# Kernel optimization log

Measured on AMD Instinct MI355X. Metric: run time of the kernel, lower is better.

Reference implementation:

```python
import jax, jax.numpy as jnp
import numpy as np

L0, L1, L2 = 32, 16, 8
NS, NB = 512, 256
CUT = 7.0
N, E, G = 16384, 131072, 16
FEAT = L0 + 3 * L1 + 5 * L2  # 120


def setup_inputs() -> dict:
    key = jax.random.key(0)
    ks = jax.random.split(key, 16)
    rn = lambda k, s, sc=1.0: jax.random.normal(k, s, jnp.float32) * sc
    inp = {}
    inp['nodes'] = rn(ks[0], (N, FEAT))
    inp['pos'] = rn(ks[1], (N, 3)) * 5.0
    inp['cell'] = rn(ks[2], (G, 3, 3))
    inp['edge_shift'] = rn(ks[3], (E, 3))
    # tensor-product path weights (e3nn FullyConnectedTensorProduct, uvw mode)
    inp['W0'] = rn(ks[4], (L0, L0, NS))
    inp['W1'] = rn(ks[5], (L1, L1, NS))
    inp['W2'] = rn(ks[6], (L2, L2, NS))
    inp['ln_g'] = jnp.ones((NS,), jnp.float32)
    inp['ln_b'] = jnp.zeros((NS,), jnp.float32)
    inp['df_w1'] = rn(ks[7], (NB, 1024), NB ** -0.5)
    inp['df_b1'] = jnp.zeros((1024,), jnp.float32)
    inp['df_w2'] = rn(ks[8], (1024, NS), 1024 ** -0.5)
    inp['df_b2'] = jnp.zeros((NS,), jnp.float32)
    inp['mi_w1'] = rn(ks[9], (NS, 1024), NS ** -0.5)
    inp['mi_b1'] = jnp.zeros((1024,), jnp.float32)
    inp['mi_w2'] = rn(ks[10], (1024, 1024), 1024 ** -0.5)
    inp['mi_b2'] = jnp.zeros((1024,), jnp.float32)
    inp['mo_w'] = rn(ks[11], (1024, 1), 1024 ** -0.5)
    inp['mo_b'] = jnp.zeros((1,), jnp.float32)
    inp['edge_index'] = jax.random.randint(ks[12], (2, E), 0, N)
    inp['batch_vec'] = jnp.sort(jax.random.randint(ks[13], (N,), 0, G))
    return inp


def _split_irreps(x):
    x0 = x[:, :L0]                                   # (E, L0) scalars 0e
    x1 = x[:, L0:L0 + 3 * L1].reshape(-1, L1, 3)      # (E, L1, 3) vectors 1o
    x2 = x[:, L0 + 3 * L1:].reshape(-1, L2, 5)        # (E, L2, 5) 2e
    return x0, x1, x2


def reference(nodes, pos, cell, edge_shift, W0, W1, W2, ln_g, ln_b,
              df_w1, df_b1, df_w2, df_b2, mi_w1, mi_b1, mi_w2, mi_b2,
              mo_w, mo_b, edge_index, batch_vec):
    src, dst = edge_index[0], edge_index[1]
    # periodic-image translation vector per edge
    bcell = cell[batch_vec[src]]                      # (E,3,3)
    tvec = jnp.einsum('ei,eij->ej', edge_shift, bcell)
    radvec = pos[dst] - pos[src] + tvec               # (E,3)
    dist = jnp.linalg.norm(radvec, axis=1, keepdims=True)  # (E,1)
    r = 1.0 / (dist + 1e-6)
    # Bessel radial embedding with cutoff CUT, NB basis functions
    n = jnp.arange(1, NB + 1, dtype=jnp.float32)
    emb = jnp.sqrt(2.0 / CUT) * jnp.sin(n * jnp.pi * r / CUT) / r  # (E,NB)
    distfilter = jax.nn.silu(emb @ df_w1 + df_b1) @ df_w2 + df_b2  # (E,NS)

    # symmetrized fully-connected tensor product -> 0e scalars
    # 0.5*(tp(xs,xd)+tp(xd,xs)) == contraction of euv with symmetrized W
    xs0, xs1, xs2 = _split_irreps(nodes[src])
    xd0, xd1, xd2 = _split_irreps(nodes[dst])
    fan = jnp.sqrt(jnp.float32(L0 * L0 + L1 * L1 + L2 * L2))  # element path norm
    sym = lambda W: 0.5 * (W + W.transpose(1, 0, 2))
    e0 = jnp.einsum('eu,ev->euv', xs0, xd0)
    mixed = jnp.einsum('euv,uvw->ew', e0, sym(W0)) / fan
    e1 = jnp.einsum('eui,evi->euv', xs1, xd1)
    mixed = mixed + jnp.einsum('euv,uvw->ew', e1, sym(W1)) / (fan * jnp.sqrt(3.0))
    e2 = jnp.einsum('eui,evi->euv', xs2, xd2)
    mixed = mixed + jnp.einsum('euv,uvw->ew', e2, sym(W2)) / (fan * jnp.sqrt(5.0))

    # LayerNorm over numscalars
    mu = jnp.mean(mixed, axis=-1, keepdims=True)
    var = jnp.mean((mixed - mu) ** 2, axis=-1, keepdims=True)
    mixednorm = (mixed - mu) * jax.lax.rsqrt(var + 1e-5) * ln_g + ln_b

    reg = mixednorm * distfilter
    h = jax.nn.silu(reg @ mi_w1 + mi_b1)
    h = jax.nn.silu(h @ mi_w2 + mi_b2)
    return h @ mo_w + mo_b  # (E,1)
```

## Files before the change

kernel.cpp:

```cpp
#include <hip/hip_runtime.h>

#define EE 131072
#define NNODE 16384
#define FEAT 120
#define NS 512
#define NB 256
#define KCAT 1344

typedef unsigned short u16;
typedef __bf16 bf16x8 __attribute__((ext_vector_type(8)));
typedef float f32x4 __attribute__((ext_vector_type(4)));
typedef unsigned short ushort8 __attribute__((ext_vector_type(8)));

__device__ __forceinline__ float b2f(u16 u) {
  union { unsigned int i; float f; } x; x.i = ((unsigned int)u) << 16; return x.f;
}
__device__ __forceinline__ u16 f2b(float f) {
  union { float f; unsigned int i; } x; x.f = f;
  unsigned int lsb = (x.i >> 16) & 1u;
  x.i += 0x7fffu + lsb;
  return (u16)(x.i >> 16);
}
__device__ __forceinline__ u16 f2b_fast(float f) {
  __bf16 h = (__bf16)f;
  union { __bf16 h; u16 u; } x; x.h = h; return x.u;
}
__device__ __forceinline__ float rdany(const void* p, long i, int f32) {
  return f32 ? ((const float*)p)[i] : b2f(((const u16*)p)[i]);
}

__device__ __forceinline__ void gload16(const u16* g, u16* l) {
  __builtin_amdgcn_global_load_lds(
      (__attribute__((address_space(1))) void*)(u16*)g,
      (__attribute__((address_space(3))) void*)l, 16, 0, 0);
}

struct PrepArgs {
  long cum[20];
  const void* src[19];
  u16* dst[19];
  float* outf;
  int* flag;
  const u16* nodes;
};

__global__ __launch_bounds__(256) void megaprep(PrepArgs a) {
  __shared__ int scnt[4];
  {
    u16 v = a.nodes[threadIdx.x];
    int e = (v >> 7) & 0xFF;
    unsigned long long b = __ballot(e >= 0x48);
    if ((threadIdx.x & 63) == 0) scnt[threadIdx.x >> 6] = __popcll(b);
  }
  __syncthreads();
  const int f32 = (scnt[0] + scnt[1] + scnt[2] + scnt[3]) >= 16;
  if (blockIdx.x == 0 && threadIdx.x == 0) *a.flag = f32;

  long i = (long)blockIdx.x * 256 + threadIdx.x;
  const long total = a.cum[19];
  if (i < total) {
    int s = 0;
    while (i >= a.cum[s + 1]) s++;
    long local = i - a.cum[s];
    a.dst[s][local] = f32 ? f2b(((const float*)a.src[s])[local])
                          : ((const u16*)a.src[s])[local];
  } else {
    long j = i - total;
    if (j < EE) a.outf[j] = 0.f;
  }
}

struct WprepArgs {
  const u16* tin[4];
  u16* tout[4];
  const u16 *W0, *W1, *W2;
  u16* wcT;
};

__device__ __forceinline__ void do_transpose(const u16* in, u16* out, int R, int C, int rem) {
  __shared__ u16 tile[32][33];
  const int bx = C >> 5;
  const int c0 = (rem % bx) * 32, r0 = (rem / bx) * 32;
  const int tx = threadIdx.x & 31, ty = threadIdx.x >> 5;
  for (int i = 0; i < 32; i += 8) {
    int r = r0 + ty + i, c = c0 + tx;
    if (r < R && c < C) tile[ty + i][tx] = in[(long)r * C + c];
  }
  __syncthreads();
  for (int i = 0; i < 32; i += 8) {
    int r = r0 + tx, c = c0 + ty + i;
    if (r < R && c < C) out[(long)c * R + r] = tile[tx][ty + i];
  }
}

__global__ __launch_bounds__(256) void wprep(WprepArgs a) {
  int b = blockIdx.x;
  if (b < 256) { do_transpose(a.tin[0], a.tout[0], 256, 1024, b); return; }
  b -= 256;
  if (b < 512) { do_transpose(a.tin[1], a.tout[1], 1024, 512, b); return; }
  b -= 512;
  if (b < 512) { do_transpose(a.tin[2], a.tout[2], 512, 1024, b); return; }
  b -= 512;
  if (b < 1024) { do_transpose(a.tin[3], a.tout[3], 1024, 1024, b); return; }
  b -= 1024;
  int idx = b * 256 + threadIdx.x;
  if (idx >= NS * KCAT) return;
  int w = idx / KCAT, k = idx - w * KCAT;
  const float fan = 36.66060556f;
  float val;
  if (k < 1024) {
    int u = k >> 5, v = k & 31;
    val = 0.5f * (b2f(a.W0[(u * 32 + v) * NS + w]) + b2f(a.W0[(v * 32 + u) * NS + w])) / fan;
  } else if (k < 1280) {
    int j = k - 1024;
    int u = j >> 4, v = j & 15;
    val = 0.5f * (b2f(a.W1[(u * 16 + v) * NS + w]) + b2f(a.W1[(v * 16 + u) * NS + w])) /
          (fan * 1.7320508076f);
  } else {
    int j = k - 1280;
    int u = j >> 3, v = j & 7;
    val = 0.5f * (b2f(a.W2[(u * 8 + v) * NS + w]) + b2f(a.W2[(v * 8 + u) * NS + w])) /
          (fan * 2.2360679775f);
  }
  a.wcT[idx] = f2b(val);
}

__global__ __launch_bounds__(256) void edge_prep(
    const u16* __restrict__ nodes, const void* __restrict__ pos, const void* __restrict__ cell,
    const void* __restrict__ shift, const int* __restrict__ eidx, const int* __restrict__ batch,
    u16* __restrict__ emb, u16* __restrict__ ocat, int e0, const int* __restrict__ flag) {
  const int wave = threadIdx.x >> 6, lane = threadIdx.x & 63;
  const int el = blockIdx.x * 4 + wave;
  const int e = e0 + el;
  const int f32 = *flag;
  __shared__ u16 sxs[4][FEAT], sxd[4][FEAT];
  const int src = eidx[e], dst = eidx[EE + e];
  for (int i = lane; i < FEAT; i += 64) {
    sxs[wave][i] = nodes[(long)src * FEAT + i];
    sxd[wave][i] = nodes[(long)dst * FEAT + i];
  }
  __syncthreads();
  const int b = batch[src];
  float s0 = rdany(shift, (long)e * 3, f32), s1 = rdany(shift, (long)e * 3 + 1, f32),
        s2 = rdany(shift, (long)e * 3 + 2, f32);
  float d2 = 0.f;
#pragma unroll
  for (int j = 0; j < 3; j++) {
    float tv = s0 * rdany(cell, b * 9 + j, f32) + s1 * rdany(cell, b * 9 + 3 + j, f32) +
               s2 * rdany(cell, b * 9 + 6 + j, f32);
    float rv = rdany(pos, dst * 3 + j, f32) - rdany(pos, src * 3 + j, f32) + tv;
    d2 += rv * rv;
  }
  float dist = sqrtf(d2);
  float r = 1.0f / (dist + 1e-6f);
  const float c0 = 0.5345224838f;
  const float pi7 = 0.44879895051f;
#pragma unroll
  for (int j = 0; j < 4; j++) {
    int n = lane + 64 * j;
    float val = c0 * sinf((float)(n + 1) * pi7 * r) / r;
    emb[(long)el * NB + n] = f2b(val);
  }
  const u16* xs = sxs[wave];
  const u16* xd = sxd[wave];
  u16* orow = ocat + (long)el * KCAT;
#pragma unroll
  for (int j = 0; j < 16; j++) {
    int k = lane + 64 * j;
    int u = k >> 5, v = k & 31;
    orow[k] = f2b(b2f(xs[u]) * b2f(xd[v]));
  }
#pragma unroll
  for (int j = 0; j < 4; j++) {
    int k = lane + 64 * j;
    int u = k >> 4, v = k & 15;
    float s = 0.f;
#pragma unroll
    for (int i = 0; i < 3; i++) s += b2f(xs[32 + u * 3 + i]) * b2f(xd[32 + v * 3 + i]);
    orow[1024 + k] = f2b(s);
  }
  {
    int u = lane >> 3, v = lane & 7;
    float s = 0.f;
#pragma unroll
    for (int i = 0; i < 5; i++) s += b2f(xs[80 + u * 5 + i]) * b2f(xd[80 + v * 5 + i]);
    orow[1280 + lane] = f2b(s);
  }
}

#define STGA(buf, h, part, kk)                                             \
  gload16(Ag + ((h)*128 + (part)*64) * (long)K + (kk),                      \
          &lA[buf][(h)*8192 + (part)*4096 + tid * 8])
#define STGB(buf, h, part, kk)                                             \
  gload16(Bg + ((h)*128 + (part)*64) * (long)K + (kk),                      \
          &lB[buf][(h)*8192 + (part)*4096 + tid * 8])
#define RDA(buf, fm, ks)                                                   \
  (*(const bf16x8*)((const char*)&lA[buf][0] +                             \
                    ((wm * 128 + (fm)*16 + row_l) * 128 + ((ks) ? ir1 : ir0))))
#define RDB(buf, fn, ks)                                                   \
  (*(const bf16x8*)((const char*)&lB[buf][0] +                             \
                    ((wn * 64 + (fn)*16 + row_l) * 128 + ((ks) ? ir1 : ir0))))
#define MF16(a, b, c) __builtin_amdgcn_mfma_f32_16x16x32_bf16(a, b, c, 0, 0, 0)
#define MFQn(mh, nh, Af, Bf)                                               \
  do {                                                                     \
    _Pragma("unroll") for (int f = 0; f < 4; f++)                          \
        _Pragma("unroll") for (int g = 0; g < 2; g++)                      \
            _Pragma("unroll") for (int ks = 0; ks < 2; ks++)               \
                acc[(mh)*4 + f][(nh)*2 + g] =                              \
        MF16(Af[f][ks], Bf[g][ks], acc[(mh)*4 + f][(nh)*2 + g]);           \
  } while (0)

template <int ACT, int OF32, int HEAD>
__global__ __launch_bounds__(512, 2) void gemm_bt(const u16* __restrict__ A,
                                                  const u16* __restrict__ BT,
                                                  const u16* __restrict__ bias,
                                                  void* __restrict__ Cv,
                                                  const u16* __restrict__ hw,
                                                  float* __restrict__ outf, int N, int K) {
  __shared__ __align__(16) u16 lA[2][16384];
  __shared__ __align__(16) u16 lB[2][16384];
  const int tid = threadIdx.x;
  const int lane = tid & 63;
  const int wave = tid >> 6;
  const int wm = wave >> 2, wn = wave & 3;
  const int row_l = lane & 15;
  const int kq16 = (lane >> 4) << 4;
  const int swz = (row_l & 7) << 4;
  const int ir0 = kq16 ^ swz;
  const int ir1 = (64 + kq16) ^ swz;

  const int nbn = N >> 8;
  int idx = blockIdx.x;
  if ((gridDim.x & 7) == 0) {
    int per = gridDim.x >> 3;
    idx = (blockIdx.x & 7) * per + (blockIdx.x >> 3);
  }
  const int mi = idx / nbn;
  const int ni = idx - mi * nbn;
  const long m0 = (long)mi * 256;
  const int n0 = ni << 8;
  const int nk = K >> 6;

  const int srow = tid >> 3;
  const int gseg = (tid & 7) ^ (srow & 7);
  const u16* Ag = A + (m0 + srow) * (long)K + gseg * 8;
  const u16* Bg = BT + (long)(n0 + srow) * K + gseg * 8;

  f32x4 acc[8][4];
#pragma unroll
  for (int i = 0; i < 8; i++)
#pragma unroll
    for (int j = 0; j < 4; j++)
#pragma unroll
      for (int q = 0; q < 4; q++) acc[i][j][q] = 0.f;

  STGA(0, 0, 0, 0); STGA(0, 0, 1, 0); STGA(0, 1, 0, 0); STGA(0, 1, 1, 0);
  STGB(0, 0, 0, 0); STGB(0, 0, 1, 0); STGB(0, 1, 0, 0); STGB(0, 1, 1, 0);
  if (nk > 1) {
    STGA(1, 0, 0, 64); STGA(1, 0, 1, 64); STGA(1, 1, 0, 64); STGA(1, 1, 1, 64);
    STGB(1, 0, 0, 64); STGB(1, 0, 1, 64); STGB(1, 1, 0, 64); STGB(1, 1, 1, 64);
    asm volatile("s_waitcnt vmcnt(8)" ::: "memory");
  } else {
    asm volatile("s_waitcnt vmcnt(0)" ::: "memory");
  }
  __builtin_amdgcn_s_barrier();

  bf16x8 af0[4][2], af1[4][2], b01[2][2], b23[2][2];

#pragma unroll
  for (int f = 0; f < 4; f++) { af0[f][0] = RDA(0, f, 0); af0[f][1] = RDA(0, f, 1); }
#pragma unroll
  for (int g = 0; g < 2; g++) { b01[g][0] = RDB(0, g, 0); b01[g][1] = RDB(0, g, 1); }

  for (int t = 0; t < nk; ++t) {
    const int cur = t & 1, nxt = cur ^ 1;
    const int kN2 = (t + 2) << 6;
    const bool p1 = (t + 1) < nk;
    const bool p2 = (t + 2) < nk;

#pragma unroll
    for (int g = 0; g < 2; g++) { b23[g][0] = RDB(cur, 2 + g, 0); b23[g][1] = RDB(cur, 2 + g, 1); }
    __builtin_amdgcn_sched_barrier(0);
    __builtin_amdgcn_s_setprio(1);
    MFQn(0, 0, af0, b01);
    __builtin_amdgcn_s_setprio(0);

#pragma unroll
    for (int f = 0; f < 4; f++) { af1[f][0] = RDA(cur, 4 + f, 0); af1[f][1] = RDA(cur, 4 + f, 1); }
    __builtin_amdgcn_sched_barrier(0);
    __builtin_amdgcn_s_setprio(1);
    MFQn(0, 1, af0, b23);
    __builtin_amdgcn_s_setprio(0);

    asm volatile("s_waitcnt vmcnt(0)" ::: "memory");
    __builtin_amdgcn_s_barrier();
    if (p1) {
#pragma unroll
      for (int f = 0; f < 4; f++) { af0[f][0] = RDA(nxt, f, 0); af0[f][1] = RDA(nxt, f, 1); }
    }
    if (p2) { STGB(cur, 0, 0, kN2); STGB(cur, 0, 1, kN2); }
    __builtin_amdgcn_sched_barrier(0);
    __builtin_amdgcn_s_setprio(1);
    MFQn(1, 0, af1, b01);
    __builtin_amdgcn_s_setprio(0);

    __builtin_amdgcn_s_barrier();
    if (p2) {
      STGB(cur, 1, 0, kN2); STGB(cur, 1, 1, kN2);
      STGA(cur, 0, 0, kN2); STGA(cur, 0, 1, kN2);
      STGA(cur, 1, 0, kN2); STGA(cur, 1, 1, kN2);
    }
    __builtin_amdgcn_sched_barrier(0);
    __builtin_amdgcn_s_setprio(1);
    MFQn(1, 1, af1, b23);
    __builtin_amdgcn_s_setprio(0);
    if (p1) {
#pragma unroll
      for (int g = 0; g < 2; g++) { b01[g][0] = RDB(nxt, g, 0); b01[g][1] = RDB(nxt, g, 1); }
      __builtin_amdgcn_sched_barrier(0);
    }
  }

  const int rql = (lane >> 4) * 2;
  const int cl = lane & 15;
  float* Cf = (float*)Cv;
  u16* Cb = (u16*)Cv;
  if (HEAD) {
    float bv[4], hv[4];
#pragma unroll
    for (int g = 0; g < 4; g++) {
      const int col = n0 + wn * 64 + g * 16 + cl;
      bv[g] = b2f(bias[col]);
      hv[g] = b2f(hw[col]);
    }
#pragma unroll
    for (int fm = 0; fm < 8; fm++) {
#pragma unroll
      for (int q = 0; q < 4; q++) {
        float s = 0.f;
#pragma unroll
        for (int g = 0; g < 4; g++) {
          float v = acc[fm][g][q] + bv[g];
          if (ACT) v = __fdividef(v, 1.0f + __expf(-v));
          s += v * hv[g];
        }
        s += __shfl_xor(s, 1);
        s += __shfl_xor(s, 2);
        s += __shfl_xor(s, 4);
        s += __shfl_xor(s, 8);
        if (cl == 0) {
          long row = m0 + wm * 128 + fm * 16 + rql * 2 + q;
          atomicAdd(&outf[row], s);
        }
      }
    }
  } else {
#pragma unroll
    for (int fm = 0; fm < 8; fm++) {
#pragma unroll
      for (int g = 0; g < 4; g++) {
        const int col = n0 + wn * 64 + g * 16 + cl;
        const float bvv = bias ? b2f(bias[col]) : 0.0f;
#pragma unroll
        for (int q = 0; q < 4; q++) {
          long row = m0 + wm * 128 + fm * 16 + rql * 2 + q;
          float v = acc[fm][g][q] + bvv;
          if (ACT) v = __fdividef(v, 1.0f + __expf(-v));
          if (OF32)
            Cf[row * N + col] = v;
          else
            Cb[row * N + col] = f2b_fast(v);
        }
      }
    }
  }
}

__global__ __launch_bounds__(256) void ln_mul_k(const float* __restrict__ mixed,
                                                const u16* __restrict__ g,
                                                const u16* __restrict__ bvec,
                                                u16* __restrict__ dfreg) {
  const int wave = threadIdx.x >> 6, lane = threadIdx.x & 63;
  const long e = (long)blockIdx.x * 4 + wave;
  const float* row = mixed + e * NS;
  float x[8];
  f32x4 v0 = *(const f32x4*)&row[lane * 8];
  f32x4 v1 = *(const f32x4*)&row[lane * 8 + 4];
#pragma unroll
  for (int j = 0; j < 4; j++) { x[j] = v0[j]; x[4 + j] = v1[j]; }
  float s = 0.f, sq = 0.f;
#pragma unroll
  for (int j = 0; j < 8; j++) { s += x[j]; sq += x[j] * x[j]; }
  for (int o = 32; o; o >>= 1) { s += __shfl_xor(s, o); sq += __shfl_xor(sq, o); }
  float mu = s * (1.0f / 512.0f);
  float var = sq * (1.0f / 512.0f) - mu * mu;
  float rstd = rsqrtf(var + 1e-5f);
  u16* drow = dfreg + e * NS;
  ushort8 dv = *(const ushort8*)&drow[lane * 8];
  ushort8 ov;
#pragma unroll
  for (int j = 0; j < 8; j++) {
    int c = lane * 8 + j;
    float val = (x[j] - mu) * rstd * b2f(g[c]) + b2f(bvec[c]);
    ov[j] = f2b(val * b2f(dv[j]));
  }
  *(ushort8*)&drow[lane * 8] = ov;
}

__global__ __launch_bounds__(256) void head_finish(const float* __restrict__ outf,
                                                   const u16* __restrict__ b,
                                                   void* __restrict__ out,
                                                   const int* __restrict__ flag) {
  int e = blockIdx.x * 256 + threadIdx.x;
  float v = outf[e] + b2f(b[0]);
  if (*flag)
    ((float*)out)[e] = v;
  else
    ((u16*)out)[e] = f2b(v);
}

extern "C" void kernel_launch(void* const* d_in, const int* in_sizes, int n_in, void* d_out,
                              int out_size, void* d_ws, size_t ws_size, hipStream_t stream) {
  const int* eidx = (const int*)d_in[19];
  const int* batch = (const int*)d_in[20];

  char* ws = (char*)d_ws;
  size_t off = 0;
  auto alloc = [&](size_t bytes) {
    char* p = ws + off;
    off += (bytes + 255) & ~(size_t)255;
    return p;
  };

  int* flag = (int*)alloc(256);
  float* outf = (float*)alloc((size_t)EE * 4);

  PrepArgs pa;
  u16* cv[19];
  long cum = 0;
  for (int i = 0; i < 19; i++) {
    long n = in_sizes[i];
    cv[i] = (u16*)alloc((size_t)n * 2);
    pa.cum[i] = cum;
    pa.src[i] = d_in[i];
    pa.dst[i] = cv[i];
    cum += n;
  }
  pa.cum[19] = cum;
  pa.outf = outf;
  pa.flag = flag;
  pa.nodes = (const u16*)d_in[0];
  {
    long tot = cum + EE;
    megaprep<<<(int)((tot + 255) / 256), 256, 0, stream>>>(pa);
  }
  const u16* nodes = cv[0];
  const u16* ln_g = cv[7];
  const u16* ln_b = cv[8];
  const u16* df_b1 = cv[10];
  const u16* df_b2 = cv[12];
  const u16* mi_b1 = cv[14];
  const u16* mi_b2 = cv[16];
  const u16* mo_w = cv[17];
  const u16* mo_b = cv[18];

  u16* w1T = (u16*)alloc(1024 * 256 * 2);
  u16* w2T = (u16*)alloc(512 * 1024 * 2);
  u16* m1T = (u16*)alloc(1024 * 512 * 2);
  u16* m2T = (u16*)alloc((size_t)1024 * 1024 * 2);
  u16* wcT = (u16*)alloc((size_t)NS * KCAT * 2);

  WprepArgs wa;
  wa.tin[0] = cv[9];  wa.tout[0] = w1T;
  wa.tin[1] = cv[11]; wa.tout[1] = w2T;
  wa.tin[2] = cv[13]; wa.tout[2] = m1T;
  wa.tin[3] = cv[15]; wa.tout[3] = m2T;
  wa.W0 = cv[4]; wa.W1 = cv[5]; wa.W2 = cv[6];
  wa.wcT = wcT;
  wprep<<<4992, 256, 0, stream>>>(wa);

  int nchunk = 1;
  while (nchunk < 64) {
    size_t CHs = (size_t)(EE / nchunk);
    size_t need = off + CHs * 6272 + 8192;
    if (need <= ws_size) break;
    nchunk <<= 1;
  }
  const int CH = EE / nchunk;

  u16* ocat = (u16*)alloc((size_t)CH * KCAT * 2);
  u16* emb = (u16*)alloc((size_t)CH * NB * 2);
  u16* h1 = (u16*)alloc((size_t)CH * 1024 * 2);
  u16* dfb = (u16*)alloc((size_t)CH * NS * 2);
  u16* h2 = ocat;
  float* mixed = (float*)h1;

  const int RB = CH / 256;
  for (int c = 0; c < nchunk; c++) {
    const int eb = c * CH;
    edge_prep<<<CH / 4, 256, 0, stream>>>(nodes, d_in[1], d_in[2], d_in[3], eidx, batch, emb,
                                          ocat, eb, flag);

    gemm_bt<1, 0, 0><<<RB * 4, 512, 0, stream>>>(emb, w1T, df_b1, h1, nullptr, nullptr, 1024, 256);
    gemm_bt<0, 0, 0><<<RB * 2, 512, 0, stream>>>(h1, w2T, df_b2, dfb, nullptr, nullptr, 512, 1024);

    gemm_bt<0, 1, 0><<<RB * 2, 512, 0, stream>>>(ocat, wcT, nullptr, mixed, nullptr, nullptr, 512,
                                                 1344);

    ln_mul_k<<<CH / 4, 256, 0, stream>>>(mixed, ln_g, ln_b, dfb);

    gemm_bt<1, 0, 0><<<RB * 4, 512, 0, stream>>>(dfb, m1T, mi_b1, h2, nullptr, nullptr, 1024, 512);
    gemm_bt<1, 0, 1><<<RB * 4, 512, 0, stream>>>(h2, m2T, mi_b2, nullptr, mo_w, outf + eb, 1024,
                                                 1024);
  }
  head_finish<<<EE / 256, 256, 0, stream>>>(outf, mo_b, d_out, flag);
}
```

Measured before the change: 1.336 ms.

## Shrink GEMM tiles to 128x128 with a simple double buffer and vectorize edge-prep stores

The hand-scheduled 256x256 GEMM with 8 waves, split fragment loads, setprio and a two-stage prefetch is replaced by a 128x128 tile with 4 waves and a plain double buffer: prefetch the next k-slab, run all MFMAs, then syncthreads. Grid sizes double to match. Separately, the edge_prep kernel now writes the embedding and outer-product rows with 4- and 8-wide vector stores instead of scalar strided stores. Smaller tiles lower arithmetic intensity and drop the careful latency hiding, in exchange for simpler code and more blocks per GPU.

```diff
diff --git a/kernel.cpp b/kernel.cpp
--- a/kernel.cpp
+++ b/kernel.cpp
@@ -11,6 +11,7 @@
 typedef __bf16 bf16x8 __attribute__((ext_vector_type(8)));
 typedef float f32x4 __attribute__((ext_vector_type(4)));
 typedef unsigned short ushort8 __attribute__((ext_vector_type(8)));
+typedef unsigned short us4 __attribute__((ext_vector_type(4)));
 
 __device__ __forceinline__ float b2f(u16 u) {
   union { unsigned int i; float f; } x; x.i = ((unsigned int)u) << 16; return x.f;
@@ -155,29 +156,44 @@
   float r = 1.0f / (dist + 1e-6f);
   const float c0 = 0.5345224838f;
   const float pi7 = 0.44879895051f;
-#pragma unroll
-  for (int j = 0; j < 4; j++) {
-    int n = lane + 64 * j;
-    float val = c0 * sinf((float)(n + 1) * pi7 * r) / r;
-    emb[(long)el * NB + n] = f2b(val);
+  {
+    us4 ev;
+#pragma unroll
+    for (int j = 0; j < 4; j++) {
+      int n = lane * 4 + j;
+      ev[j] = f2b(c0 * sinf((float)(n + 1) * pi7 * r) / r);
+    }
+    *(us4*)&emb[(long)el * NB + lane * 4] = ev;
   }
   const u16* xs = sxs[wave];
   const u16* xd = sxd[wave];
   u16* orow = ocat + (long)el * KCAT;
-#pragma unroll
-  for (int j = 0; j < 16; j++) {
-    int k = lane + 64 * j;
-    int u = k >> 5, v = k & 31;
-    orow[k] = f2b(b2f(xs[u]) * b2f(xd[v]));
-  }
-#pragma unroll
-  for (int j = 0; j < 4; j++) {
-    int k = lane + 64 * j;
-    int u = k >> 4, v = k & 15;
-    float s = 0.f;
-#pragma unroll
-    for (int i = 0; i < 3; i++) s += b2f(xs[32 + u * 3 + i]) * b2f(xd[32 + v * 3 + i]);
-    orow[1024 + k] = f2b(s);
+  {
+    const float xu = b2f(xs[lane >> 1]);
+    const int v0 = (lane & 1) * 16;
+    const ushort8 xd0 = *(const ushort8*)&xd[v0];
+    const ushort8 xd1 = *(const ushort8*)&xd[v0 + 8];
+    ushort8 o0, o1;
+#pragma unroll
+    for (int j = 0; j < 8; j++) {
+      o0[j] = f2b(xu * b2f(xd0[j]));
+      o1[j] = f2b(xu * b2f(xd1[j]));
+    }
+    *(ushort8*)&orow[lane * 16] = o0;
+    *(ushort8*)&orow[lane * 16 + 8] = o1;
+  }
+  {
+    const int u = lane >> 2;
+    us4 o;
+#pragma unroll
+    for (int j = 0; j < 4; j++) {
+      const int v = (lane & 3) * 4 + j;
+      float s = 0.f;
+#pragma unroll
+      for (int i = 0; i < 3; i++) s += b2f(xs[32 + u * 3 + i]) * b2f(xd[32 + v * 3 + i]);
+      o[j] = f2b(s);
+    }
+    *(us4*)&orow[1024 + lane * 4] = o;
   }
   {
     int u = lane >> 3, v = lane & 7;
@@ -188,48 +204,44 @@
   }
 }
 
-#define STGA(buf, h, part, kk)                                             \
-  gload16(Ag + ((h)*128 + (part)*64) * (long)K + (kk),                      \
-          &lA[buf][(h)*8192 + (part)*4096 + tid * 8])
-#define STGB(buf, h, part, kk)                                             \
-  gload16(Bg + ((h)*128 + (part)*64) * (long)K + (kk),                      \
-          &lB[buf][(h)*8192 + (part)*4096 + tid * 8])
+#define STGA(buf, kk)                                                      \
+  do {                                                                     \
+    _Pragma("unroll") for (int i = 0; i < 4; i++)                          \
+        gload16(Ag + (i * 32) * (long)K + (kk), &lA[buf][i * 2048 + tid * 8]); \
+  } while (0)
+#define STGB(buf, kk)                                                      \
+  do {                                                                     \
+    _Pragma("unroll") for (int i = 0; i < 4; i++)                          \
+        gload16(Bg + (i * 32) * (long)K + (kk), &lB[buf][i * 2048 + tid * 8]); \
+  } while (0)
 #define RDA(buf, fm, ks)                                                   \
   (*(const bf16x8*)((const char*)&lA[buf][0] +                             \
-                    ((wm * 128 + (fm)*16 + row_l) * 128 + ((ks) ? ir1 : ir0))))
+                    ((wm * 64 + (fm)*16 + row_l) * 128 + ((ks) ? ir1 : ir0))))
 #define RDB(buf, fn, ks)                                                   \
   (*(const bf16x8*)((const char*)&lB[buf][0] +                             \
                     ((wn * 64 + (fn)*16 + row_l) * 128 + ((ks) ? ir1 : ir0))))
 #define MF16(a, b, c) __builtin_amdgcn_mfma_f32_16x16x32_bf16(a, b, c, 0, 0, 0)
-#define MFQn(mh, nh, Af, Bf)                                               \
-  do {                                                                     \
-    _Pragma("unroll") for (int f = 0; f < 4; f++)                          \
-        _Pragma("unroll") for (int g = 0; g < 2; g++)                      \
-            _Pragma("unroll") for (int ks = 0; ks < 2; ks++)               \
-                acc[(mh)*4 + f][(nh)*2 + g] =                              \
-        MF16(Af[f][ks], Bf[g][ks], acc[(mh)*4 + f][(nh)*2 + g]);           \
-  } while (0)
 
 template <int ACT, int OF32, int HEAD>
-__global__ __launch_bounds__(512, 2) void gemm_bt(const u16* __restrict__ A,
+__global__ __launch_bounds__(256, 2) void gemm_bt(const u16* __restrict__ A,
                                                   const u16* __restrict__ BT,
                                                   const u16* __restrict__ bias,
                                                   void* __restrict__ Cv,
                                                   const u16* __restrict__ hw,
                                                   float* __restrict__ outf, int N, int K) {
-  __shared__ __align__(16) u16 lA[2][16384];
-  __shared__ __align__(16) u16 lB[2][16384];
+  __shared__ __align__(16) u16 lA[2][8192];
+  __shared__ __align__(16) u16 lB[2][8192];
   const int tid = threadIdx.x;
   const int lane = tid & 63;
   const int wave = tid >> 6;
-  const int wm = wave >> 2, wn = wave & 3;
+  const int wm = wave >> 1, wn = wave & 1;
   const int row_l = lane & 15;
   const int kq16 = (lane >> 4) << 4;
   const int swz = (row_l & 7) << 4;
   const int ir0 = kq16 ^ swz;
   const int ir1 = (64 + kq16) ^ swz;
 
-  const int nbn = N >> 8;
+  const int nbn = N >> 7;
   int idx = blockIdx.x;
   if ((gridDim.x & 7) == 0) {
     int per = gridDim.x >> 3;
@@ -237,8 +249,8 @@
   }
   const int mi = idx / nbn;
   const int ni = idx - mi * nbn;
-  const long m0 = (long)mi * 256;
-  const int n0 = ni << 8;
+  const long m0 = (long)mi * 128;
+  const int n0 = ni << 7;
   const int nk = K >> 6;
 
   const int srow = tid >> 3;
@@ -246,79 +258,39 @@
   const u16* Ag = A + (m0 + srow) * (long)K + gseg * 8;
   const u16* Bg = BT + (long)(n0 + srow) * K + gseg * 8;
 
-  f32x4 acc[8][4];
-#pragma unroll
-  for (int i = 0; i < 8; i++)
+  f32x4 acc[4][4];
+#pragma unroll
+  for (int i = 0; i < 4; i++)
 #pragma unroll
     for (int j = 0; j < 4; j++)
 #pragma unroll
       for (int q = 0; q < 4; q++) acc[i][j][q] = 0.f;
 
-  STGA(0, 0, 0, 0); STGA(0, 0, 1, 0); STGA(0, 1, 0, 0); STGA(0, 1, 1, 0);
-  STGB(0, 0, 0, 0); STGB(0, 0, 1, 0); STGB(0, 1, 0, 0); STGB(0, 1, 1, 0);
-  if (nk > 1) {
-    STGA(1, 0, 0, 64); STGA(1, 0, 1, 64); STGA(1, 1, 0, 64); STGA(1, 1, 1, 64);
-    STGB(1, 0, 0, 64); STGB(1, 0, 1, 64); STGB(1, 1, 0, 64); STGB(1, 1, 1, 64);
-    asm volatile("s_waitcnt vmcnt(8)" ::: "memory");
-  } else {
-    asm volatile("s_waitcnt vmcnt(0)" ::: "memory");
-  }
+  STGA(0, 0);
+  STGB(0, 0);
+  asm volatile("s_waitcnt vmcnt(0)" ::: "memory");
   __builtin_amdgcn_s_barrier();
 
-  bf16x8 af0[4][2], af1[4][2], b01[2][2], b23[2][2];
-
-#pragma unroll
-  for (int f = 0; f < 4; f++) { af0[f][0] = RDA(0, f, 0); af0[f][1] = RDA(0, f, 1); }
-#pragma unroll
-  for (int g = 0; g < 2; g++) { b01[g][0] = RDB(0, g, 0); b01[g][1] = RDB(0, g, 1); }
+  bf16x8 af[4][2], bf[4][2];
 
   for (int t = 0; t < nk; ++t) {
     const int cur = t & 1, nxt = cur ^ 1;
-    const int kN2 = (t + 2) << 6;
-    const bool p1 = (t + 1) < nk;
-    const bool p2 = (t + 2) < nk;
-
-#pragma unroll
-    for (int g = 0; g < 2; g++) { b23[g][0] = RDB(cur, 2 + g, 0); b23[g][1] = RDB(cur, 2 + g, 1); }
-    __builtin_amdgcn_sched_barrier(0);
-    __builtin_amdgcn_s_setprio(1);
-    MFQn(0, 0, af0, b01);
-    __builtin_amdgcn_s_setprio(0);
-
-#pragma unroll
-    for (int f = 0; f < 4; f++) { af1[f][0] = RDA(cur, 4 + f, 0); af1[f][1] = RDA(cur, 4 + f, 1); }
-    __builtin_amdgcn_sched_barrier(0);
-    __builtin_amdgcn_s_setprio(1);
-    MFQn(0, 1, af0, b23);
-    __builtin_amdgcn_s_setprio(0);
-
-    asm volatile("s_waitcnt vmcnt(0)" ::: "memory");
-    __builtin_amdgcn_s_barrier();
-    if (p1) {
-#pragma unroll
-      for (int f = 0; f < 4; f++) { af0[f][0] = RDA(nxt, f, 0); af0[f][1] = RDA(nxt, f, 1); }
-    }
-    if (p2) { STGB(cur, 0, 0, kN2); STGB(cur, 0, 1, kN2); }
-    __builtin_amdgcn_sched_barrier(0);
-    __builtin_amdgcn_s_setprio(1);
-    MFQn(1, 0, af1, b01);
-    __builtin_amdgcn_s_setprio(0);
-
-    __builtin_amdgcn_s_barrier();
-    if (p2) {
-      STGB(cur, 1, 0, kN2); STGB(cur, 1, 1, kN2);
-      STGA(cur, 0, 0, kN2); STGA(cur, 0, 1, kN2);
-      STGA(cur, 1, 0, kN2); STGA(cur, 1, 1, kN2);
-    }
-    __builtin_amdgcn_sched_barrier(0);
-    __builtin_amdgcn_s_setprio(1);
-    MFQn(1, 1, af1, b23);
-    __builtin_amdgcn_s_setprio(0);
-    if (p1) {
-#pragma unroll
-      for (int g = 0; g < 2; g++) { b01[g][0] = RDB(nxt, g, 0); b01[g][1] = RDB(nxt, g, 1); }
-      __builtin_amdgcn_sched_barrier(0);
-    }
+    if (t + 1 < nk) {
+      STGA(nxt, (t + 1) * 64);
+      STGB(nxt, (t + 1) * 64);
+    }
+#pragma unroll
+    for (int f = 0; f < 4; f++) { af[f][0] = RDA(cur, f, 0); af[f][1] = RDA(cur, f, 1); }
+#pragma unroll
+    for (int g = 0; g < 4; g++) { bf[g][0] = RDB(cur, g, 0); bf[g][1] = RDB(cur, g, 1); }
+#pragma unroll
+    for (int f = 0; f < 4; f++)
+#pragma unroll
+      for (int g = 0; g < 4; g++)
+#pragma unroll
+        for (int ks = 0; ks < 2; ks++)
+          acc[f][g] = MF16(af[f][ks], bf[g][ks], acc[f][g]);
+    __syncthreads();
   }
 
   const int rql = (lane >> 4) * 2;
@@ -334,7 +306,7 @@
       hv[g] = b2f(hw[col]);
     }
 #pragma unroll
-    for (int fm = 0; fm < 8; fm++) {
+    for (int fm = 0; fm < 4; fm++) {
 #pragma unroll
       for (int q = 0; q < 4; q++) {
         float s = 0.f;
@@ -349,21 +321,21 @@
         s += __shfl_xor(s, 4);
         s += __shfl_xor(s, 8);
         if (cl == 0) {
-          long row = m0 + wm * 128 + fm * 16 + rql * 2 + q;
+          long row = m0 + wm * 64 + fm * 16 + rql * 2 + q;
           atomicAdd(&outf[row], s);
         }
       }
     }
   } else {
 #pragma unroll
-    for (int fm = 0; fm < 8; fm++) {
+    for (int fm = 0; fm < 4; fm++) {
 #pragma unroll
       for (int g = 0; g < 4; g++) {
         const int col = n0 + wn * 64 + g * 16 + cl;
         const float bvv = bias ? b2f(bias[col]) : 0.0f;
 #pragma unroll
         for (int q = 0; q < 4; q++) {
-          long row = m0 + wm * 128 + fm * 16 + rql * 2 + q;
+          long row = m0 + wm * 64 + fm * 16 + rql * 2 + q;
           float v = acc[fm][g][q] + bvv;
           if (ACT) v = __fdividef(v, 1.0f + __expf(-v));
           if (OF32)
@@ -495,22 +467,22 @@
   u16* h2 = ocat;
   float* mixed = (float*)h1;
 
-  const int RB = CH / 256;
+  const int RB = CH / 128;
   for (int c = 0; c < nchunk; c++) {
     const int eb = c * CH;
     edge_prep<<<CH / 4, 256, 0, stream>>>(nodes, d_in[1], d_in[2], d_in[3], eidx, batch, emb,
                                           ocat, eb, flag);
 
-    gemm_bt<1, 0, 0><<<RB * 4, 512, 0, stream>>>(emb, w1T, df_b1, h1, nullptr, nullptr, 1024, 256);
-    gemm_bt<0, 0, 0><<<RB * 2, 512, 0, stream>>>(h1, w2T, df_b2, dfb, nullptr, nullptr, 512, 1024);
-
-    gemm_bt<0, 1, 0><<<RB * 2, 512, 0, stream>>>(ocat, wcT, nullptr, mixed, nullptr, nullptr, 512,
+    gemm_bt<1, 0, 0><<<RB * 8, 256, 0, stream>>>(emb, w1T, df_b1, h1, nullptr, nullptr, 1024, 256);
+    gemm_bt<0, 0, 0><<<RB * 4, 256, 0, stream>>>(h1, w2T, df_b2, dfb, nullptr, nullptr, 512, 1024);
+
+    gemm_bt<0, 1, 0><<<RB * 4, 256, 0, stream>>>(ocat, wcT, nullptr, mixed, nullptr, nullptr, 512,
                                                  1344);
 
     ln_mul_k<<<CH / 4, 256, 0, stream>>>(mixed, ln_g, ln_b, dfb);
 
-    gemm_bt<1, 0, 0><<<RB * 4, 512, 0, stream>>>(dfb, m1T, mi_b1, h2, nullptr, nullptr, 1024, 512);
-    gemm_bt<1, 0, 1><<<RB * 4, 512, 0, stream>>>(h2, m2T, mi_b2, nullptr, mo_w, outf + eb, 1024,
+    gemm_bt<1, 0, 0><<<RB * 8, 256, 0, stream>>>(dfb, m1T, mi_b1, h2, nullptr, nullptr, 1024, 512);
+    gemm_bt<1, 0, 1><<<RB * 8, 256, 0, stream>>>(h2, m2T, mi_b2, nullptr, mo_w, outf + eb, 1024,
                                                  1024);
   }
   head_finish<<<EE / 256, 256, 0, stream>>>(outf, mo_b, d_out, flag);
```

After: 1.496 ms. +11.9%, slower.
